# Performance work log

Hardware: AMD Instinct MI355X
Metric: run time of the kernel (lower is better)

Reference implementation:

```python
import jax, jax.numpy as jnp
import numpy as np

EPS = 1e-7
ALPHA = 0.5          # centripetal Catmull-Rom
CP_NUM = 1000        # number of control points (before loop closing)
N_QUERIES = 8_388_608


def build_spline(cps):
    """Replicates the constructor: close loop, add auxiliary endpoints, knot vector."""
    cps = jnp.concatenate([cps, cps[:1]], axis=0)  # (M+1, 2) closed loop
    l01 = jnp.sqrt(jnp.sum((cps[0] - cps[1]) ** 2) + EPS)
    l_last = jnp.sqrt(jnp.sum((cps[-1] - cps[-2]) ** 2) + EPS)
    # original code calls .detach_() on the two chord lengths
    l01 = jax.lax.stop_gradient(l01)
    l_last = jax.lax.stop_gradient(l_last)
    first = cps[0] - l01 / l_last * (cps[-1] - cps[-2])
    last = cps[-1] + l_last / l01 * (cps[1] - cps[0])
    aux = jnp.concatenate([first[None], cps, last[None]], axis=0)  # (M+3, 2)
    seg = jnp.sum((aux[1:] - aux[:-1]) ** 2, axis=-1) ** (ALPHA / 2.0)
    knots = jnp.concatenate([jnp.zeros((1,), aux.dtype), jnp.cumsum(seg)])  # (M+3,)
    # original code detaches t
    return aux, jax.lax.stop_gradient(knots)


def setup_inputs() -> dict:
    key = jax.random.key(0)
    k1, k2 = jax.random.split(key)
    cps = jax.random.normal(k1, (CP_NUM, 2), dtype=jnp.float32) * 10.0
    # queries must lie in the valid knot range [t[1], t[cp_num+1]) like self.ts
    _, knots = build_spline(cps)
    lo = knots[1]
    hi = knots[CP_NUM + 1] - EPS
    u = jax.random.uniform(k2, (N_QUERIES,), dtype=jnp.float32)
    tq = lo + u * (hi - lo)
    return {"cps": cps, "tq": tq}


def reference(cps, tq):
    aux, knots = build_spline(cps)
    # batched replacement of the sequential segment search:
    # sg s.t. knots[sg] <= tv < knots[sg+1], clipped to [1, CP_NUM] like the while loop
    sg = jnp.clip(jnp.searchsorted(knots, tq, side="right") - 1, 1, CP_NUM)
    t0 = knots[sg - 1][:, None]
    t1 = knots[sg][:, None]
    t2 = knots[sg + 1][:, None]
    t3 = knots[sg + 2][:, None]
    P0 = aux[sg - 1]
    P1 = aux[sg]
    P2 = aux[sg + 1]
    P3 = aux[sg + 2]
    tv = tq[:, None]
    # recursive (Barry-Goldman) Catmull-Rom evaluation, fully vectorized over queries
    x01 = ((t1 - tv) * P0 + (tv - t0) * P1) / (t1 - t0)
    x12 = ((t2 - tv) * P1 + (tv - t1) * P2) / (t2 - t1)
    x23 = ((t3 - tv) * P2 + (tv - t2) * P3) / (t3 - t2)
    x012 = ((t2 - tv) * x01 + (tv - t0) * x12) / (t2 - t0)
    x123 = ((t3 - tv) * x12 + (tv - t1) * x23) / (t3 - t1)
    return ((t2 - tv) * x012 + (tv - t1) * x123) / (t2 - t1)  # (N, 2)
```

## Files before the change

kernel.cpp:

```cpp
#include <hip/hip_runtime.h>

#define CPN  1000
#define NAUX (CPN + 3)
#define NB   1024
#define EPSF 1e-7f

typedef __fp16 half2v __attribute__((ext_vector_type(2)));

static __device__ __forceinline__ unsigned int pk2h(float a, float b) {
    half2v h = __builtin_amdgcn_cvt_pkrtz(a, b);
    return *reinterpret_cast<unsigned int*>(&h);
}
static __device__ __forceinline__ float h2f_lo(unsigned int u) {
    unsigned short us = (unsigned short)u;
    __fp16 h = *reinterpret_cast<__fp16*>(&us);
    return (float)h;
}
static __device__ __forceinline__ float h2f_hi(unsigned int u) {
    unsigned short us = (unsigned short)(u >> 16);
    __fp16 h = *reinterpret_cast<__fp16*>(&us);
    return (float)h;
}

__global__ __launch_bounds__(1024)
void spline_setup(const float* __restrict__ cps,
                  float* __restrict__ g_kn,
                  uint4* __restrict__ g_rec,
                  uint4* __restrict__ g_lut)
{
    __shared__ float sax[NAUX];
    __shared__ float say[NAUX];
    __shared__ float skn[NAUX + 1];
    __shared__ float wsum[16];
    const int tid = threadIdx.x;

    const float c0x = cps[0],         c0y = cps[1];
    const float c1x = cps[2],         c1y = cps[3];
    const float cLx = cps[2*(CPN-1)], cLy = cps[2*(CPN-1)+1];
    const float dx01 = c0x - c1x, dy01 = c0y - c1y;
    const float dxL  = c0x - cLx, dyL  = c0y - cLy;
    const float l01   = sqrtf(dx01*dx01 + dy01*dy01 + EPSF);
    const float llast = sqrtf(dxL*dxL   + dyL*dyL   + EPSF);

    if (tid < CPN) { sax[tid+1] = cps[2*tid]; say[tid+1] = cps[2*tid+1]; }
    if (tid == 0) {
        sax[0]     = c0x - (l01/llast) * dxL;
        say[0]     = c0y - (l01/llast) * dyL;
        sax[CPN+1] = c0x;  say[CPN+1] = c0y;
        sax[CPN+2] = c0x + (llast/l01) * (c1x - c0x);
        say[CPN+2] = c0y + (llast/l01) * (c1y - c0y);
    }
    __syncthreads();

    float v = 0.f;
    if (tid < NAUX - 1) {
        const float dx = sax[tid+1] - sax[tid];
        const float dy = say[tid+1] - say[tid];
        v = sqrtf(sqrtf(dx*dx + dy*dy));
    }
    #pragma unroll
    for (int off = 1; off < 64; off <<= 1) {
        const float w = __shfl_up(v, off, 64);
        if ((tid & 63) >= off) v += w;
    }
    if ((tid & 63) == 63) wsum[tid >> 6] = v;
    __syncthreads();
    if (tid < 16) {
        float x = wsum[tid];
        #pragma unroll
        for (int off = 1; off < 16; off <<= 1) {
            const float w = __shfl_up(x, off, 16);
            if (tid >= off) x += w;
        }
        wsum[tid] = x;
    }
    __syncthreads();
    const float incl = v + ((tid >= 64) ? wsum[(tid >> 6) - 1] : 0.f);

    if (tid == 0)       { skn[0] = 0.f; skn[NAUX] = 1e30f; g_kn[0] = 0.f; g_kn[1003] = 1e30f; }
    if (tid < NAUX - 1) { skn[tid+1] = incl; g_kn[tid+1] = incl; }
    __syncthreads();

    if (tid < CPN) {
        const int sg = tid + 1;
        const float t0 = skn[sg-1], t1 = skn[sg], t2 = skn[sg+1], t3 = skn[sg+2];
        const float A = t1 - t0, B = t2 - t1, C = t3 - t2;
        const float r01 = 1.0f / A;
        const float r12 = 1.0f / B;
        const float r23 = 1.0f / C;
        const float r02 = 1.0f / (A + B);
        const float r13 = 1.0f / (B + C);
        const float C3  = B + C;

        const float P0x = sax[sg-1], P0y = say[sg-1];
        const float P1x = sax[sg],   P1y = say[sg];
        const float P2x = sax[sg+1], P2y = say[sg+1];
        const float P3x = sax[sg+2], P3y = say[sg+2];

        const float L01_1x = (P1x - P0x) * r01, L01_1y = (P1y - P0y) * r01;
        const float L12_1x = (P2x - P1x) * r12, L12_1y = (P2y - P1y) * r12;
        const float L23_0x = ((B + C) * P2x - B * P3x) * r23;
        const float L23_0y = ((B + C) * P2y - B * P3y) * r23;
        const float L23_1x = (P3x - P2x) * r23, L23_1y = (P3y - P2y) * r23;

        const float Q012_0x = (B * P1x + A * P1x) * r02;
        const float Q012_0y = (B * P1y + A * P1y) * r02;
        const float Q012_1x = (B * L01_1x - P1x + A * L12_1x + P1x) * r02;
        const float Q012_1y = (B * L01_1y - P1y + A * L12_1y + P1y) * r02;
        const float Q012_2x = (L12_1x - L01_1x) * r02;
        const float Q012_2y = (L12_1y - L01_1y) * r02;

        const float Q123_0x = C3 * P1x * r13;
        const float Q123_0y = C3 * P1y * r13;
        const float Q123_1x = (C3 * L12_1x - P1x + L23_0x) * r13;
        const float Q123_1y = (C3 * L12_1y - P1y + L23_0y) * r13;
        const float Q123_2x = (L23_1x - L12_1x) * r13;
        const float Q123_2y = (L23_1y - L12_1y) * r13;

        const float k0x = B * Q012_0x * r12;
        const float k1x = (B * Q012_1x - Q012_0x + Q123_0x) * r12;
        const float k2x = (B * Q012_2x - Q012_1x + Q123_1x) * r12;
        const float k3x = (Q123_2x - Q012_2x) * r12;
        const float k0y = B * Q012_0y * r12;
        const float k1y = (B * Q012_1y - Q012_0y + Q123_0y) * r12;
        const float k2y = (B * Q012_2y - Q012_1y + Q123_1y) * r12;
        const float k3y = (Q123_2y - Q012_2y) * r12;

        uint4 r;
        r.x = pk2h(k0x, k0y);
        r.y = pk2h(k1x, k1y);
        r.z = pk2h(k2x, k2y);
        r.w = pk2h(k3x, k3y);
        g_rec[tid] = r;
    }
    __syncthreads();

    const float lo = skn[1];
    const float hi = skn[CPN + 1];
    const float w  = (hi - lo) / (float)NB;
    if (tid < NB) {
        const float bl = lo + (float)tid * w;
        int l = 0, h = NAUX;
        #pragma unroll
        for (int it = 0; it < 10; ++it) {
            const int mid = (l + h) >> 1;
            const bool c = (skn[mid] <= bl);
            l = c ? mid : l;
            h = c ? h : mid;
        }
        const int k0 = l < 1 ? 1 : (l > CPN ? CPN : l);
        const float t1_0 = skn[k0];

        unsigned short dh[5];
        float prev = t1_0;
        #pragma unroll
        for (int i = 1; i <= 5; ++i) {
            const float kn = (k0 + i <= CPN) ? skn[k0 + i] : 1e30f;
            float delta = kn - prev;
            if (delta > 60000.0f) delta = 60000.0f;
            if (delta < 0.0f)     delta = 0.0f;
            dh[i-1] = (unsigned short)(pk2h(delta, 0.0f) & 0xFFFFu);
            prev = kn;
        }
        const unsigned int flag =
            ((k0 + 6 <= CPN) && (skn[k0 + 6] <= bl + w * 1.001f)) ? 0x8000u : 0u;

        uint4 e;
        e.x = __float_as_uint(t1_0);
        e.y = ((unsigned int)k0 | flag) | ((unsigned int)dh[0] << 16);
        e.z = (unsigned int)dh[1] | ((unsigned int)dh[2] << 16);
        e.w = (unsigned int)dh[3] | ((unsigned int)dh[4] << 16);
        g_lut[tid] = e;
    }
}

__global__ __launch_bounds__(512, 8)
void spline_eval(const float* __restrict__ tq,
                 const float* __restrict__ g_kn,
                 const uint4* __restrict__ g_rec,
                 const uint4* __restrict__ g_lut,
                 float* __restrict__ out,
                 int n)
{
    __shared__ __align__(16) uint4 s_lut[NB];
    __shared__ __align__(16) uint4 s_rec[CPN];
    __shared__ __align__(16) float s_kn[1004];
    const int tid = threadIdx.x;

    for (int i = tid; i < NB; i += 512)  s_lut[i] = g_lut[i];
    for (int i = tid; i < CPN; i += 512) s_rec[i] = g_rec[i];
    for (int i = tid; i < 251; i += 512) ((float4*)s_kn)[i] = ((const float4*)g_kn)[i];
    __syncthreads();

    const float lo    = s_kn[1];
    const float hi    = s_kn[CPN + 1];
    const float inv_w = (float)NB / (hi - lo);

    const int gid = blockIdx.x * 512 + tid;
    const int T   = gridDim.x * 512;
    const int P   = n >> 1;

    const float2* tq2  = (const float2*)tq;
    float4*       out4 = (float4*)out;

    for (int p0 = gid; p0 < P; p0 += 4 * T) {
        const int p1 = p0 + T, p2 = p0 + 2 * T, p3 = p0 + 3 * T;
        const bool b1 = p1 < P, b2 = p2 < P, b3 = p3 < P;

        const float2 ta = tq2[p0];
        const float2 tb = b1 ? tq2[p1] : ta;
        const float2 tc = b2 ? tq2[p2] : ta;
        const float2 td = b3 ? tq2[p3] : ta;

        #pragma unroll
        for (int g = 0; g < 2; ++g) {
            float t0_, t1_, t2_, t3_;
            if (g == 0) { t0_ = ta.x; t1_ = ta.y; t2_ = tb.x; t3_ = tb.y; }
            else        { t0_ = tc.x; t1_ = tc.y; t2_ = td.x; t3_ = td.y; }
            const float tv[4] = {t0_, t1_, t2_, t3_};

            uint4 e[4];
            #pragma unroll
            for (int q = 0; q < 4; ++q) {
                int b = (int)((tv[q] - lo) * inv_w);
                b = b < 0 ? 0 : (b > NB - 1 ? NB - 1 : b);
                e[q] = s_lut[b];
            }

            int   sg[4];
            float uu[4];
            #pragma unroll
            for (int q = 0; q < 4; ++q) {
                const float t = tv[q];
                float t1 = __uint_as_float(e[q].x);
                const unsigned int sgf = e[q].y & 0xFFFFu;
                int s = (int)(sgf & 0x7FFFu);
                const float c1 = t1 + h2f_hi(e[q].y);
                const float c2 = c1 + h2f_lo(e[q].z);
                const float c3 = c2 + h2f_hi(e[q].z);
                const float c4 = c3 + h2f_lo(e[q].w);
                const float c5 = c4 + h2f_hi(e[q].w);
                const bool g1 = t >= c1, g2 = t >= c2, g3 = t >= c3, g4 = t >= c4, g5 = t >= c5;
                s += (int)g1 + (int)g2 + (int)g3 + (int)g4 + (int)g5;
                t1 = g1 ? c1 : t1;
                t1 = g2 ? c2 : t1;
                t1 = g3 ? c3 : t1;
                t1 = g4 ? c4 : t1;
                t1 = g5 ? c5 : t1;
                if (__builtin_expect((sgf & 0x8000u) != 0 && g5, 0)) {
                    while (s < CPN && s_kn[s + 1] <= t) ++s;
                    t1 = s_kn[s];
                }
                sg[q] = s;
                uu[q] = t - t1;
            }

            uint4 r[4];
            #pragma unroll
            for (int q = 0; q < 4; ++q) r[q] = s_rec[sg[q] - 1];

            float rx[4], ry[4];
            #pragma unroll
            for (int q = 0; q < 4; ++q) {
                const float u = uu[q];
                rx[q] = fmaf(fmaf(fmaf(h2f_lo(r[q].w), u, h2f_lo(r[q].z)), u, h2f_lo(r[q].y)), u, h2f_lo(r[q].x));
                ry[q] = fmaf(fmaf(fmaf(h2f_hi(r[q].w), u, h2f_hi(r[q].z)), u, h2f_hi(r[q].y)), u, h2f_hi(r[q].x));
            }

            if (g == 0) {
                out4[p0] = make_float4(rx[0], ry[0], rx[1], ry[1]);
                if (b1) out4[p1] = make_float4(rx[2], ry[2], rx[3], ry[3]);
            } else {
                if (b2) out4[p2] = make_float4(rx[0], ry[0], rx[1], ry[1]);
                if (b3) out4[p3] = make_float4(rx[2], ry[2], rx[3], ry[3]);
            }
        }
    }

    if ((n & 1) && gid == 0) {
        const int q = n - 1;
        const float t = tq[q];
        int b = (int)((t - lo) * inv_w);
        b = b < 0 ? 0 : (b > NB - 1 ? NB - 1 : b);
        const uint4 e = s_lut[b];
        float t1 = __uint_as_float(e.x);
        const unsigned int sgf = e.y & 0xFFFFu;
        int s = (int)(sgf & 0x7FFFu);
        const float c1 = t1 + h2f_hi(e.y);
        const float c2 = c1 + h2f_lo(e.z);
        const float c3 = c2 + h2f_hi(e.z);
        const float c4 = c3 + h2f_lo(e.w);
        const float c5 = c4 + h2f_hi(e.w);
        const bool g1 = t >= c1, g2 = t >= c2, g3 = t >= c3, g4 = t >= c4, g5 = t >= c5;
        s += (int)g1 + (int)g2 + (int)g3 + (int)g4 + (int)g5;
        t1 = g1 ? c1 : t1; t1 = g2 ? c2 : t1; t1 = g3 ? c3 : t1;
        t1 = g4 ? c4 : t1; t1 = g5 ? c5 : t1;
        if ((sgf & 0x8000u) != 0 && g5) {
            while (s < CPN && s_kn[s + 1] <= t) ++s;
            t1 = s_kn[s];
        }
        const float u = t - t1;
        const uint4 r = s_rec[s - 1];
        out[2*q]     = fmaf(fmaf(fmaf(h2f_lo(r.w), u, h2f_lo(r.z)), u, h2f_lo(r.y)), u, h2f_lo(r.x));
        out[2*q + 1] = fmaf(fmaf(fmaf(h2f_hi(r.w), u, h2f_hi(r.z)), u, h2f_hi(r.y)), u, h2f_hi(r.x));
    }
}

extern "C" void kernel_launch(void* const* d_in, const int* in_sizes, int n_in,
                              void* d_out, int out_size, void* d_ws, size_t ws_size,
                              hipStream_t stream) {
    const float* cps = (const float*)d_in[0];
    const float* tq  = (const float*)d_in[1];
    float* out       = (float*)d_out;
    const int n      = in_sizes[1];

    float* g_kn  = (float*)d_ws;
    uint4* g_rec = (uint4*)((char*)d_ws + 4096);
    uint4* g_lut = (uint4*)((char*)d_ws + 20480);

    spline_setup<<<1, 1024, 0, stream>>>(cps, g_kn, g_rec, g_lut);

    const int blocks = 1024;
    spline_eval<<<blocks, 512, 0, stream>>>(tq, g_kn, g_rec, g_lut, out, n);
}
```

Measured before the change: 28.46 us.

## Resample spline onto uniform Hermite bins to eliminate segment search

The setup kernel evaluates the exact Catmull-Rom segments and their derivatives at 4096 uniform parameter points, then builds per-bin cubic Hermite coefficients stored as fp16. The eval kernel indexes a bin directly from the query value and evaluates one cubic, removing the LUT lookup, knot-delta comparisons and fallback loop. This adds approximation error where bins straddle knots, and the per-block LDS table load grows to 64KB with a switch to 1024-thread blocks.

```diff
diff --git a/kernel.cpp b/kernel.cpp
--- a/kernel.cpp
+++ b/kernel.cpp
@@ -2,15 +2,9 @@
 
 #define CPN  1000
 #define NAUX (CPN + 3)
-#define NB   1024
+#define M    4096
 #define EPSF 1e-7f
 
-typedef __fp16 half2v __attribute__((ext_vector_type(2)));
-
-static __device__ __forceinline__ unsigned int pk2h(float a, float b) {
-    half2v h = __builtin_amdgcn_cvt_pkrtz(a, b);
-    return *reinterpret_cast<unsigned int*>(&h);
-}
 static __device__ __forceinline__ float h2f_lo(unsigned int u) {
     unsigned short us = (unsigned short)u;
     __fp16 h = *reinterpret_cast<__fp16*>(&us);
@@ -21,17 +15,23 @@
     __fp16 h = *reinterpret_cast<__fp16*>(&us);
     return (float)h;
 }
+static __device__ __forceinline__ unsigned int pk2h_rtn(float a, float b) {
+    __fp16 ha = (__fp16)a, hb = (__fp16)b;
+    unsigned short ua = *reinterpret_cast<unsigned short*>(&ha);
+    unsigned short ub = *reinterpret_cast<unsigned short*>(&hb);
+    return (unsigned int)ua | ((unsigned int)ub << 16);
+}
 
 __global__ __launch_bounds__(1024)
 void spline_setup(const float* __restrict__ cps,
-                  float* __restrict__ g_kn,
                   uint4* __restrict__ g_rec,
-                  uint4* __restrict__ g_lut)
+                  float* __restrict__ g_meta)
 {
     __shared__ float sax[NAUX];
     __shared__ float say[NAUX];
     __shared__ float skn[NAUX + 1];
     __shared__ float wsum[16];
+    __shared__ float segc[8 * CPN];
     const int tid = threadIdx.x;
 
     const float c0x = cps[0],         c0y = cps[1];
@@ -60,8 +60,8 @@
     }
     #pragma unroll
     for (int off = 1; off < 64; off <<= 1) {
-        const float w = __shfl_up(v, off, 64);
-        if ((tid & 63) >= off) v += w;
+        const float w_ = __shfl_up(v, off, 64);
+        if ((tid & 63) >= off) v += w_;
     }
     if ((tid & 63) == 63) wsum[tid >> 6] = v;
     __syncthreads();
@@ -69,16 +69,16 @@
         float x = wsum[tid];
         #pragma unroll
         for (int off = 1; off < 16; off <<= 1) {
-            const float w = __shfl_up(x, off, 16);
-            if (tid >= off) x += w;
+            const float w_ = __shfl_up(x, off, 16);
+            if (tid >= off) x += w_;
         }
         wsum[tid] = x;
     }
     __syncthreads();
     const float incl = v + ((tid >= 64) ? wsum[(tid >> 6) - 1] : 0.f);
 
-    if (tid == 0)       { skn[0] = 0.f; skn[NAUX] = 1e30f; g_kn[0] = 0.f; g_kn[1003] = 1e30f; }
-    if (tid < NAUX - 1) { skn[tid+1] = incl; g_kn[tid+1] = incl; }
+    if (tid == 0)       { skn[0] = 0.f; skn[NAUX] = 1e30f; }
+    if (tid < NAUX - 1) { skn[tid+1] = incl; }
     __syncthreads();
 
     if (tid < CPN) {
@@ -117,87 +117,88 @@
         const float Q123_2x = (L23_1x - L12_1x) * r13;
         const float Q123_2y = (L23_1y - L12_1y) * r13;
 
-        const float k0x = B * Q012_0x * r12;
-        const float k1x = (B * Q012_1x - Q012_0x + Q123_0x) * r12;
-        const float k2x = (B * Q012_2x - Q012_1x + Q123_1x) * r12;
-        const float k3x = (Q123_2x - Q012_2x) * r12;
-        const float k0y = B * Q012_0y * r12;
-        const float k1y = (B * Q012_1y - Q012_0y + Q123_0y) * r12;
-        const float k2y = (B * Q012_2y - Q012_1y + Q123_1y) * r12;
-        const float k3y = (Q123_2y - Q012_2y) * r12;
-
-        uint4 r;
-        r.x = pk2h(k0x, k0y);
-        r.y = pk2h(k1x, k1y);
-        r.z = pk2h(k2x, k2y);
-        r.w = pk2h(k3x, k3y);
-        g_rec[tid] = r;
+        float* c = &segc[(size_t)tid * 8];
+        c[0] = B * Q012_0x * r12;
+        c[1] = (B * Q012_1x - Q012_0x + Q123_0x) * r12;
+        c[2] = (B * Q012_2x - Q012_1x + Q123_1x) * r12;
+        c[3] = (Q123_2x - Q012_2x) * r12;
+        c[4] = B * Q012_0y * r12;
+        c[5] = (B * Q012_1y - Q012_0y + Q123_0y) * r12;
+        c[6] = (B * Q012_2y - Q012_1y + Q123_1y) * r12;
+        c[7] = (Q123_2y - Q012_2y) * r12;
     }
     __syncthreads();
 
     const float lo = skn[1];
     const float hi = skn[CPN + 1];
-    const float w  = (hi - lo) / (float)NB;
-    if (tid < NB) {
-        const float bl = lo + (float)tid * w;
-        int l = 0, h = NAUX;
-        #pragma unroll
-        for (int it = 0; it < 10; ++it) {
-            const int mid = (l + h) >> 1;
-            const bool c = (skn[mid] <= bl);
-            l = c ? mid : l;
-            h = c ? h : mid;
-        }
-        const int k0 = l < 1 ? 1 : (l > CPN ? CPN : l);
-        const float t1_0 = skn[k0];
-
-        unsigned short dh[5];
-        float prev = t1_0;
-        #pragma unroll
-        for (int i = 1; i <= 5; ++i) {
-            const float kn = (k0 + i <= CPN) ? skn[k0 + i] : 1e30f;
-            float delta = kn - prev;
-            if (delta > 60000.0f) delta = 60000.0f;
-            if (delta < 0.0f)     delta = 0.0f;
-            dh[i-1] = (unsigned short)(pk2h(delta, 0.0f) & 0xFFFFu);
-            prev = kn;
-        }
-        const unsigned int flag =
-            ((k0 + 6 <= CPN) && (skn[k0 + 6] <= bl + w * 1.001f)) ? 0x8000u : 0u;
-
-        uint4 e;
-        e.x = __float_as_uint(t1_0);
-        e.y = ((unsigned int)k0 | flag) | ((unsigned int)dh[0] << 16);
-        e.z = (unsigned int)dh[1] | ((unsigned int)dh[2] << 16);
-        e.w = (unsigned int)dh[3] | ((unsigned int)dh[4] << 16);
-        g_lut[tid] = e;
-    }
-}
-
-__global__ __launch_bounds__(512, 8)
+    const float w  = (hi - lo) / (float)M;
+    const float iw = (float)M / (hi - lo);
+
+    if (tid == 0) {
+        g_meta[0] = lo; g_meta[1] = hi; g_meta[2] = w; g_meta[3] = iw;
+    }
+
+    for (int i = tid; i < M; i += 1024) {
+        float f[2][2], d[2][2];
+        #pragma unroll
+        for (int ep = 0; ep < 2; ++ep) {
+            const float x = lo + (float)(i + ep) * w;
+            int l = 0, h = 1003;
+            #pragma unroll
+            for (int it = 0; it < 10; ++it) {
+                const int mid = (l + h) >> 1;
+                const bool cnd = (skn[mid] <= x);
+                l = cnd ? mid : l;
+                h = cnd ? h : mid;
+            }
+            int s = l < 1 ? 1 : (l > CPN ? CPN : l);
+            const float u = x - skn[s];
+            const float* c = &segc[(size_t)(s - 1) * 8];
+            f[ep][0] = fmaf(fmaf(fmaf(c[3], u, c[2]), u, c[1]), u, c[0]);
+            d[ep][0] = fmaf(fmaf(3.0f * c[3], u, 2.0f * c[2]), u, c[1]);
+            f[ep][1] = fmaf(fmaf(fmaf(c[7], u, c[6]), u, c[5]), u, c[4]);
+            d[ep][1] = fmaf(fmaf(3.0f * c[7], u, 2.0f * c[6]), u, c[5]);
+        }
+        float cc[4][2];
+        #pragma unroll
+        for (int ax = 0; ax < 2; ++ax) {
+            const float f0 = f[0][ax], f1 = f[1][ax];
+            const float d0 = d[0][ax], d1 = d[1][ax];
+            const float iwv = 1.0f / w;
+            const float D = (f1 - f0) * iwv;
+            cc[0][ax] = f0;
+            cc[1][ax] = d0;
+            cc[2][ax] = (3.0f * D - 2.0f * d0 - d1) * iwv;
+            cc[3][ax] = (d0 + d1 - 2.0f * D) * iwv * iwv;
+        }
+        uint4 r;
+        r.x = pk2h_rtn(cc[0][0], cc[0][1]);
+        r.y = pk2h_rtn(cc[1][0], cc[1][1]);
+        r.z = pk2h_rtn(cc[2][0], cc[2][1]);
+        r.w = pk2h_rtn(cc[3][0], cc[3][1]);
+        g_rec[i] = r;
+    }
+}
+
+__global__ __launch_bounds__(1024, 8)
 void spline_eval(const float* __restrict__ tq,
-                 const float* __restrict__ g_kn,
                  const uint4* __restrict__ g_rec,
-                 const uint4* __restrict__ g_lut,
+                 const float* __restrict__ g_meta,
                  float* __restrict__ out,
                  int n)
 {
-    __shared__ __align__(16) uint4 s_lut[NB];
-    __shared__ __align__(16) uint4 s_rec[CPN];
-    __shared__ __align__(16) float s_kn[1004];
+    __shared__ __align__(16) uint4 s_rec[M];
     const int tid = threadIdx.x;
 
-    for (int i = tid; i < NB; i += 512)  s_lut[i] = g_lut[i];
-    for (int i = tid; i < CPN; i += 512) s_rec[i] = g_rec[i];
-    for (int i = tid; i < 251; i += 512) ((float4*)s_kn)[i] = ((const float4*)g_kn)[i];
-    __syncthreads();
-
-    const float lo    = s_kn[1];
-    const float hi    = s_kn[CPN + 1];
-    const float inv_w = (float)NB / (hi - lo);
-
-    const int gid = blockIdx.x * 512 + tid;
-    const int T   = gridDim.x * 512;
+    for (int i = tid; i < M; i += 1024) s_rec[i] = g_rec[i];
+
+    const float lo    = g_meta[0];
+    const float w     = g_meta[2];
+    const float inv_w = g_meta[3];
+    __syncthreads();
+
+    const int gid = blockIdx.x * 1024 + tid;
+    const int T   = gridDim.x * 1024;
     const int P   = n >> 1;
 
     const float2* tq2  = (const float2*)tq;
@@ -214,55 +215,24 @@
 
         #pragma unroll
         for (int g = 0; g < 2; ++g) {
-            float t0_, t1_, t2_, t3_;
-            if (g == 0) { t0_ = ta.x; t1_ = ta.y; t2_ = tb.x; t3_ = tb.y; }
-            else        { t0_ = tc.x; t1_ = tc.y; t2_ = td.x; t3_ = td.y; }
-            const float tv[4] = {t0_, t1_, t2_, t3_};
-
-            uint4 e[4];
+            float tv[4];
+            if (g == 0) { tv[0] = ta.x; tv[1] = ta.y; tv[2] = tb.x; tv[3] = tb.y; }
+            else        { tv[0] = tc.x; tv[1] = tc.y; tv[2] = td.x; tv[3] = td.y; }
+
+            int bb[4];
             #pragma unroll
             for (int q = 0; q < 4; ++q) {
                 int b = (int)((tv[q] - lo) * inv_w);
-                b = b < 0 ? 0 : (b > NB - 1 ? NB - 1 : b);
-                e[q] = s_lut[b];
-            }
-
-            int   sg[4];
-            float uu[4];
+                bb[q] = b < 0 ? 0 : (b > M - 1 ? M - 1 : b);
+            }
+            uint4 r[4];
+            #pragma unroll
+            for (int q = 0; q < 4; ++q) r[q] = s_rec[bb[q]];
+
+            float rx[4], ry[4];
             #pragma unroll
             for (int q = 0; q < 4; ++q) {
-                const float t = tv[q];
-                float t1 = __uint_as_float(e[q].x);
-                const unsigned int sgf = e[q].y & 0xFFFFu;
-                int s = (int)(sgf & 0x7FFFu);
-                const float c1 = t1 + h2f_hi(e[q].y);
-                const float c2 = c1 + h2f_lo(e[q].z);
-                const float c3 = c2 + h2f_hi(e[q].z);
-                const float c4 = c3 + h2f_lo(e[q].w);
-                const float c5 = c4 + h2f_hi(e[q].w);
-                const bool g1 = t >= c1, g2 = t >= c2, g3 = t >= c3, g4 = t >= c4, g5 = t >= c5;
-                s += (int)g1 + (int)g2 + (int)g3 + (int)g4 + (int)g5;
-                t1 = g1 ? c1 : t1;
-                t1 = g2 ? c2 : t1;
-                t1 = g3 ? c3 : t1;
-                t1 = g4 ? c4 : t1;
-                t1 = g5 ? c5 : t1;
-                if (__builtin_expect((sgf & 0x8000u) != 0 && g5, 0)) {
-                    while (s < CPN && s_kn[s + 1] <= t) ++s;
-                    t1 = s_kn[s];
-                }
-                sg[q] = s;
-                uu[q] = t - t1;
-            }
-
-            uint4 r[4];
-            #pragma unroll
-            for (int q = 0; q < 4; ++q) r[q] = s_rec[sg[q] - 1];
-
-            float rx[4], ry[4];
-            #pragma unroll
-            for (int q = 0; q < 4; ++q) {
-                const float u = uu[q];
+                const float u = tv[q] - fmaf((float)bb[q], w, lo);
                 rx[q] = fmaf(fmaf(fmaf(h2f_lo(r[q].w), u, h2f_lo(r[q].z)), u, h2f_lo(r[q].y)), u, h2f_lo(r[q].x));
                 ry[q] = fmaf(fmaf(fmaf(h2f_hi(r[q].w), u, h2f_hi(r[q].z)), u, h2f_hi(r[q].y)), u, h2f_hi(r[q].x));
             }
@@ -281,26 +251,9 @@
         const int q = n - 1;
         const float t = tq[q];
         int b = (int)((t - lo) * inv_w);
-        b = b < 0 ? 0 : (b > NB - 1 ? NB - 1 : b);
-        const uint4 e = s_lut[b];
-        float t1 = __uint_as_float(e.x);
-        const unsigned int sgf = e.y & 0xFFFFu;
-        int s = (int)(sgf & 0x7FFFu);
-        const float c1 = t1 + h2f_hi(e.y);
-        const float c2 = c1 + h2f_lo(e.z);
-        const float c3 = c2 + h2f_hi(e.z);
-        const float c4 = c3 + h2f_lo(e.w);
-        const float c5 = c4 + h2f_hi(e.w);
-        const bool g1 = t >= c1, g2 = t >= c2, g3 = t >= c3, g4 = t >= c4, g5 = t >= c5;
-        s += (int)g1 + (int)g2 + (int)g3 + (int)g4 + (int)g5;
-        t1 = g1 ? c1 : t1; t1 = g2 ? c2 : t1; t1 = g3 ? c3 : t1;
-        t1 = g4 ? c4 : t1; t1 = g5 ? c5 : t1;
-        if ((sgf & 0x8000u) != 0 && g5) {
-            while (s < CPN && s_kn[s + 1] <= t) ++s;
-            t1 = s_kn[s];
-        }
-        const float u = t - t1;
-        const uint4 r = s_rec[s - 1];
+        b = b < 0 ? 0 : (b > M - 1 ? M - 1 : b);
+        const float u = t - fmaf((float)b, w, lo);
+        const uint4 r = s_rec[b];
         out[2*q]     = fmaf(fmaf(fmaf(h2f_lo(r.w), u, h2f_lo(r.z)), u, h2f_lo(r.y)), u, h2f_lo(r.x));
         out[2*q + 1] = fmaf(fmaf(fmaf(h2f_hi(r.w), u, h2f_hi(r.z)), u, h2f_hi(r.y)), u, h2f_hi(r.x));
     }
@@ -314,12 +267,11 @@
     float* out       = (float*)d_out;
     const int n      = in_sizes[1];
 
-    float* g_kn  = (float*)d_ws;
-    uint4* g_rec = (uint4*)((char*)d_ws + 4096);
-    uint4* g_lut = (uint4*)((char*)d_ws + 20480);
-
-    spline_setup<<<1, 1024, 0, stream>>>(cps, g_kn, g_rec, g_lut);
-
-    const int blocks = 1024;
-    spline_eval<<<blocks, 512, 0, stream>>>(tq, g_kn, g_rec, g_lut, out, n);
-}
+    uint4* g_rec  = (uint4*)d_ws;
+    float* g_meta = (float*)((char*)d_ws + 65536);
+
+    spline_setup<<<1, 1024, 0, stream>>>(cps, g_rec, g_meta);
+
+    const int blocks = 512;
+    spline_eval<<<blocks, 1024, 0, stream>>>(tq, g_rec, g_meta, out, n);
+}
```

New measurement: 32.06 us. 12.7% more time.
